# Kernel optimization log

Measured on AMD Instinct MI355X. Metric: run time of the kernel, lower is better.

The kernel has to match this reference:

```python
import jax, jax.numpy as jnp
import numpy as np
from jax import lax

NQ = 9          # num_qubits
K = 3           # basis_size
S = 16          # max_num_snapshots
H = 128         # hidden_size
B = 16          # batch
D = 2 ** NQ

# basis_reconstruction buffer = Pauli X, Y, Z (complex64), non-trainable
PAULI = jnp.array([[[0, 1], [1, 0]],
                   [[0, -1j], [1j, 0]],
                   [[1, 0], [0, -1]]], dtype=jnp.complex64)


def setup_inputs() -> dict:
    key = jax.random.key(0)
    ks = jax.random.split(key, 11)
    return {
        "snapshot": jax.random.normal(ks[0], (B, NQ), jnp.float32),
        "basis_comp_vector": jax.random.uniform(ks[1], (B, NQ, K), dtype=jnp.float32),
        "rho": jax.random.normal(ks[2], (B, 2) + (2,) * NQ, jnp.float32),
        "h0": jax.random.normal(ks[3], (B, H), jnp.float32),
        "c0": jax.random.normal(ks[4], (B, H), jnp.float32),
        "W_ih": jax.random.normal(ks[5], (4 * H, NQ + NQ * K), jnp.float32) * 0.1,
        "W_hh": jax.random.normal(ks[6], (4 * H, H), jnp.float32) * 0.1,
        "b_ih": jax.random.normal(ks[7], (4 * H,), jnp.float32) * 0.1,
        "b_hh": jax.random.normal(ks[8], (4 * H,), jnp.float32) * 0.1,
        "Wp": jax.random.normal(ks[9], (NQ, K, H), jnp.float32) * 0.1,
        "bp": jax.random.normal(ks[10], (NQ, K), jnp.float32) * 0.1,
    }


def _lstm_cell(x, h, c, W_ih, W_hh, b_ih, b_hh):
    g = x @ W_ih.T + h @ W_hh.T + b_ih + b_hh
    i, f, gg, o = jnp.split(g, 4, axis=-1)  # torch gate order i,f,g,o
    i, f, o = jax.nn.sigmoid(i), jax.nn.sigmoid(f), jax.nn.sigmoid(o)
    c = f * c + i * jnp.tanh(gg)
    return o * jnp.tanh(c), c


def _apply_1q(psi, M, i):
    """Apply per-batch 2x2 matrix M [B,2,2] to qubit i of psi [B]+[2]*NQ."""
    psi = jnp.moveaxis(psi, 1 + i, 1)
    sh = psi.shape
    out = jnp.einsum('bij,bjr->bir', M, psi.reshape(sh[0], 2, -1))
    return jnp.moveaxis(out.reshape(sh), 1, 1 + i)


def _take_snapshots(psi, a):
    """Vectorized take_snapshot: psi [B]+[2]*NQ complex, a [B,NQ,K] real (sqrt of probs).
    For each qubit build psi_plus/psi_minus projectors, record expectation
    s = <P+> - <P-> and collapse onto the (normalized) plus branch."""
    axs = tuple(range(1, NQ + 1))
    zeros = jnp.zeros(psi.shape[0], jnp.float32)
    ss = []
    for i in range(NQ):
        a1, a2, a3 = a[:, i, 0], a[:, i, 1], a[:, i, 2]
        an = jnp.sqrt(a1 * a1 + a2 * a2 + a3 * a3)
        nrm = 1.0 / jnp.sqrt(2.0 * an * (a3 + an))
        pp = jnp.stack([lax.complex(a3 + an, zeros), lax.complex(a1, a2)], axis=-1) * nrm[:, None]
        pm = jnp.stack([lax.complex(-a1, a2), lax.complex(a3 + an, zeros)], axis=-1) * nrm[:, None]
        Pp = pp[:, :, None] * jnp.conj(pp)[:, None, :]  # [B,2,2]
        Pm = pm[:, :, None] * jnp.conj(pm)[:, None, :]
        psi_p = _apply_1q(psi, Pp, i)
        psi_m = _apply_1q(psi, Pm, i)
        prob_p = jnp.sum(psi_p.real ** 2 + psi_p.imag ** 2, axis=axs)
        prob_m = jnp.sum(psi_m.real ** 2 + psi_m.imag ** 2, axis=axs)
        ss.append(prob_p - prob_m)
        psi = psi_p / jnp.sqrt(prob_p).reshape((-1,) + (1,) * NQ)  # collapse
    return jnp.stack(ss, axis=1)  # [B,NQ]


def _bkron(A, Bm):
    b, m, n = A.shape
    p, q = Bm.shape[1], Bm.shape[2]
    return (A[:, :, None, :, None] * Bm[:, None, :, None, :]).reshape(b, m * p, n * q)


def _forward(snapshot, basis_comp_vector, rho, h0, c0, W_ih, W_hh, b_ih, b_hh, Wp, bp):
    b = snapshot.shape[0]
    psi = lax.complex(rho[:, 0], rho[:, 1])  # [B]+[2]*NQ pure state
    x = jnp.concatenate([snapshot, basis_comp_vector.reshape(b, -1)], axis=-1)
    inputs = [x]
    h, c = h0, c0
    for _ in range(S - 1):
        h, c = _lstm_cell(x, h, c, W_ih, W_hh, b_ih, b_hh)
        probs = jax.nn.softmax(jnp.einsum('bh,nkh->bnk', h, Wp) + bp, axis=-1)
        amps = jnp.sqrt(probs)  # [B,NQ,K]
        snap = _take_snapshots(psi, amps)
        x = jnp.concatenate([snap, amps.reshape(b, -1)], axis=-1)
        inputs.append(x)
    # classical-shadow reconstruction, summed over snapshots
    I2 = jnp.eye(2, dtype=jnp.complex64)
    acc = jnp.zeros((b, D, D), jnp.complex64)
    last_bv = None
    for x in inputs:
        shadow = x[:, :NQ]                                   # [B,NQ]
        bv = x[:, NQ:].reshape(b, NQ, K)
        last_bv = bv
        basis = jnp.einsum('bnk,kij->bnij', bv.astype(jnp.complex64), PAULI)
        rho_q = (I2 + shadow[:, :, None, None].astype(jnp.complex64) * basis * 3.0) / 2.0
        r = rho_q[:, 0]
        for iq in range(1, NQ):
            r = _bkron(r, rho_q[:, iq])
        acc = acc + r
    rho_rec = acc / S
    out = jnp.stack([rho_rec.real, rho_rec.imag], axis=1)  # [B,2,D,D]
    return out, last_bv


def reference(snapshot, basis_comp_vector, rho, h0, c0, W_ih, W_hh, b_ih, b_hh, Wp, bp):
    return _forward(snapshot, basis_comp_vector, rho, h0, c0,
                    W_ih, W_hh, b_ih, b_hh, Wp, bp)
```

## Files before the change

### kernel.cpp

```cpp
#include <hip/hip_runtime.h>
#include <math.h>

#define NQ 9
#define KK 3
#define S 16
#define H 128
#define BB 16
#define D 512
#define DD (D*D)

__device__ __forceinline__ float sigf(float x){ return 1.f/(1.f + __expf(-x)); }

#define DPP_ADD(x, ctrl, rmask) \
  x += __int_as_float(__builtin_amdgcn_update_dpp(0, __float_as_int(x), ctrl, rmask, 0xf, false))

__device__ __forceinline__ float wave_red_sum(float x) {
  DPP_ADD(x, 0x111, 0xf);
  DPP_ADD(x, 0x112, 0xf);
  DPP_ADD(x, 0x114, 0xf);
  DPP_ADD(x, 0x118, 0xf);
  DPP_ADD(x, 0x142, 0xa);
  DPP_ADD(x, 0x143, 0xc);
  return __int_as_float(__builtin_amdgcn_readlane(__float_as_int(x), 63));
}
#define RL(v, l) __int_as_float(__builtin_amdgcn_readlane(__float_as_int(v), (l)))
#define DPP_ROR(x, n) \
  __int_as_float(__builtin_amdgcn_update_dpp(0, __float_as_int(x), 0x120 + (n), 0xf, 0xf, false))

__global__ __launch_bounds__(512, 2)
void seq_kernel(const float* __restrict__ snapshot,
                const float* __restrict__ bcv,
                const float* __restrict__ rho,
                const float* __restrict__ h0,
                const float* __restrict__ c0,
                const float* __restrict__ W_ih,
                const float* __restrict__ W_hh,
                const float* __restrict__ b_ih,
                const float* __restrict__ b_hh,
                const float* __restrict__ Wp,
                const float* __restrict__ bp,
                float4* __restrict__ mats,
                float* __restrict__ last_bv)
{
  const int b    = blockIdx.x;
  const int tid  = threadIdx.x;
  const int lane = tid & 63;
  const int w    = tid >> 6;

  __shared__ __align__(16) float xh[164];
  __shared__ float gbuf[512];
  __shared__ float prj[27];

  float4 wih[9], whh[32];
  {
    const float4* wi = (const float4*)(W_ih + tid*36);
    #pragma unroll
    for (int k = 0; k < 9; ++k) wih[k] = wi[k];
    const float4* wh = (const float4*)(W_hh + tid*H);
    #pragma unroll
    for (int k = 0; k < 32; ++k) whh[k] = wh[k];
  }
  const float bias = b_ih[tid] + b_hh[tid];
  float2 wpv[4]; float bpv[4];
  #pragma unroll
  for (int i = 0; i < 4; ++i) {
    int u = w + 8*i;
    if (u < 27) { wpv[i] = *(const float2*)(Wp + u*H + 2*lane); bpv[i] = bp[u]; }
    else        { wpv[i] = make_float2(0.f, 0.f); bpv[i] = 0.f; }
  }

  float cc0 = c0[b*H + 2*lane], cc1 = c0[b*H + 2*lane + 1];

  float pr0[8], pi0[8], norm0 = 0.f;
  if (w == 0) {
    #pragma unroll
    for (int j = 0; j < 8; ++j) {
      pr0[j] = rho[b*1024 + j*64 + lane];
      pi0[j] = rho[b*1024 + 512 + j*64 + lane];
    }
    float ls = 0.f;
    #pragma unroll
    for (int j = 0; j < 8; ++j) ls += pr0[j]*pr0[j] + pi0[j]*pi0[j];
    norm0 = wave_red_sum(ls);
  }

  if (tid < 128) xh[36 + tid] = h0[b*H + tid];
  if (tid < NQ)  xh[tid]      = snapshot[b*NQ + tid];
  if (tid < 27)  xh[NQ + tid] = bcv[b*27 + tid];
  __syncthreads();

  if (tid < NQ) {
    float s = xh[tid], v0 = xh[9+tid*3], v1 = xh[9+tid*3+1], v2 = xh[9+tid*3+2];
    mats[(b*S + 0)*NQ + tid] = make_float4(
        0.5f*(1.f + 3.f*s*v2), 1.5f*s*v0, -1.5f*s*v1, 0.5f*(1.f - 3.f*s*v2));
  }

  for (int t = 1; t < S; ++t) {
    {
      const float4* x4 = (const float4*)xh;
      float g0 = bias, g1 = 0.f, g2 = 0.f, g3 = 0.f;
      #pragma unroll
      for (int k = 0; k < 9; ++k) {
        float4 wv = wih[k], xv = x4[k];
        g0 += wv.x*xv.x; g1 += wv.y*xv.y; g2 += wv.z*xv.z; g3 += wv.w*xv.w;
      }
      #pragma unroll
      for (int k = 0; k < 32; ++k) {
        float4 wv = whh[k], xv = x4[9 + k];
        g0 += wv.x*xv.x; g1 += wv.y*xv.y; g2 += wv.z*xv.z; g3 += wv.w*xv.w;
      }
      gbuf[tid] = (g0 + g1) + (g2 + g3);
    }
    __syncthreads();

    float h0v, h1v;
    {
      float2 gI = *(const float2*)(gbuf + 2*lane);
      float2 gF = *(const float2*)(gbuf + 128 + 2*lane);
      float2 gG = *(const float2*)(gbuf + 256 + 2*lane);
      float2 gO = *(const float2*)(gbuf + 384 + 2*lane);
      cc0 = sigf(gF.x)*cc0 + sigf(gI.x)*tanhf(gG.x);
      cc1 = sigf(gF.y)*cc1 + sigf(gI.y)*tanhf(gG.y);
      h0v = sigf(gO.x)*tanhf(cc0);
      h1v = sigf(gO.y)*tanhf(cc1);
    }
    if (w == 1) *(float2*)(xh + 36 + 2*lane) = make_float2(h0v, h1v);

    #pragma unroll
    for (int i = 0; i < 4; ++i) {
      float p = wave_red_sum(wpv[i].x*h0v + wpv[i].y*h1v);
      int u = w + 8*i;
      if (u < 27 && lane == 0) prj[u] = p + bpv[i];
    }
    __syncthreads();

    if (w == 0) {
      float a1 = 0.f, a2 = 0.f, a3 = 0.f;
      float k0v = 0.f, k1rv = 0.f, k1iv = 0.f;
      if (lane < NQ) {
        float l0 = prj[lane*3], l1 = prj[lane*3+1], l2 = prj[lane*3+2];
        float mx = fmaxf(l0, fmaxf(l1, l2));
        float e0 = __expf(l0 - mx), e1 = __expf(l1 - mx), e2 = __expf(l2 - mx);
        float inv = 1.f/(e0 + e1 + e2);
        a1 = sqrtf(e0*inv); a2 = sqrtf(e1*inv); a3 = sqrtf(e2*inv);
        float an = sqrtf(a1*a1 + a2*a2 + a3*a3);
        float t3 = a3 + an;
        float n1 = 1.f/sqrtf(2.f*an*t3);
        k0v = n1*t3; k1rv = n1*a1; k1iv = -n1*a2;
      }
      float part[9];

      float r4[4], i4[4];
      {
        const float K0 = RL(k0v,0), K1r = RL(k1rv,0), K1i = RL(k1iv,0);
        float lp = 0.f;
        #pragma unroll
        for (int j = 0; j < 4; ++j) {
          r4[j] = K0*pr0[j] + K1r*pr0[j+4] - K1i*pi0[j+4];
          i4[j] = K0*pi0[j] + K1r*pi0[j+4] + K1i*pr0[j+4];
          lp += r4[j]*r4[j] + i4[j]*i4[j];
        }
        part[0] = lp;
      }
      float r2[2], i2[2];
      {
        const float K0 = RL(k0v,1), K1r = RL(k1rv,1), K1i = RL(k1iv,1);
        float lp = 0.f;
        #pragma unroll
        for (int j = 0; j < 2; ++j) {
          r2[j] = K0*r4[j] + K1r*r4[j+2] - K1i*i4[j+2];
          i2[j] = K0*i4[j] + K1r*i4[j+2] + K1i*r4[j+2];
          lp += r2[j]*r2[j] + i2[j]*i2[j];
        }
        part[1] = lp;
      }
      float wr, wi_;
      {
        const float K0 = RL(k0v,2), K1r = RL(k1rv,2), K1i = RL(k1iv,2);
        wr  = K0*r2[0] + K1r*r2[1] - K1i*i2[1];
        wi_ = K0*i2[0] + K1r*i2[1] + K1i*r2[1];
        part[2] = wr*wr + wi_*wi_;
      }
      #pragma unroll
      for (int q = 3; q < 5; ++q) {
        const int half = 32 >> (q - 3);
        const float K0 = RL(k0v,q), K1r = RL(k1rv,q), K1i = RL(k1iv,q);
        float pr = __shfl(wr,  lane + half, 64);
        float pi = __shfl(wi_, lane + half, 64);
        float nr = K0*wr  + K1r*pr - K1i*pi;
        float ni = K0*wi_ + K1r*pi + K1i*pr;
        wr = nr; wi_ = ni;
        part[q] = (lane < half) ? (nr*nr + ni*ni) : 0.f;
      }
      #pragma unroll
      for (int q = 5; q < NQ; ++q) {
        const int half = 32 >> (q - 3);
        const float K0 = RL(k0v,q), K1r = RL(k1rv,q), K1i = RL(k1iv,q);
        float pr, pi;
        if      (q == 5) { pr = DPP_ROR(wr, 8);  pi = DPP_ROR(wi_, 8);  }
        else if (q == 6) { pr = DPP_ROR(wr, 12); pi = DPP_ROR(wi_, 12); }
        else if (q == 7) { pr = DPP_ROR(wr, 14); pi = DPP_ROR(wi_, 14); }
        else             { pr = DPP_ROR(wr, 15); pi = DPP_ROR(wi_, 15); }
        float nr = K0*wr  + K1r*pr - K1i*pi;
        float ni = K0*wi_ + K1r*pi + K1i*pr;
        wr = nr; wi_ = ni;
        part[q] = (lane < half) ? (nr*nr + ni*ni) : 0.f;
      }
      float L[9];
      #pragma unroll
      for (int q = 0; q < NQ; ++q) L[q] = wave_red_sum(part[q]);
      float sv = 2.f*L[0] - norm0;
      #pragma unroll
      for (int q = 1; q < NQ; ++q) {
        float r = 2.f*L[q]/L[q-1] - 1.f;
        sv = (lane == q) ? r : sv;
      }
      if (lane < NQ) {
        xh[lane] = sv;
        xh[9 + lane*3]     = a1;
        xh[9 + lane*3 + 1] = a2;
        xh[9 + lane*3 + 2] = a3;
        mats[(b*S + t)*NQ + lane] = make_float4(
            0.5f*(1.f + 3.f*sv*a3), 1.5f*sv*a1,
            -1.5f*sv*a2,            0.5f*(1.f - 3.f*sv*a3));
      }
    }
    __syncthreads();
  }

  if (tid < 27) last_bv[b*27 + tid] = xh[9 + tid];
}

__device__ __forceinline__ void herm_entry(float4 m, int rb, int cb, float& er, float& ei) {
  if (rb == 0) { if (cb == 0) { er = m.x; ei = 0.f; } else { er = m.y; ei = m.z; } }
  else         { if (cb == 0) { er = m.y; ei = -m.z; } else { er = m.w; ei = 0.f; } }
}

__global__ __launch_bounds__(512, 2)
void kron_kernel(const float4* __restrict__ mats_g, float* __restrict__ out)
{
  const int b   = blockIdx.y;
  const int bm  = blockIdx.x;
  const int tid = threadIdx.x;
  const int rTp = bm >> 3;
  const int rg  = bm & 7;

  __shared__ float4 matsh[S*NQ];
  __shared__ float2 top[S][2][16];
  __shared__ __align__(16) float2 bot[4][S][32];

  if (tid < S*NQ) matsh[tid] = mats_g[b*S*NQ + tid];
  __syncthreads();

  {
    int t = tid >> 5, rTi = (tid >> 4) & 1, cT = tid & 15;
    int rT = rTp*2 + rTi;
    float re = 1.f, im = 0.f;
    #pragma unroll
    for (int q = 0; q < 4; ++q) {
      int rb = (rT >> (3 - q)) & 1, cb = (cT >> (3 - q)) & 1;
      float er, ei; herm_entry(matsh[t*NQ + q], rb, cb, er, ei);
      float nr = re*er - im*ei; im = re*ei + im*er; re = nr;
    }
    top[t][rTi][cT] = make_float2(re, im);
  }
  {
    int r_ = tid >> 7, t_ = (tid >> 3) & 15, cB0 = (tid & 7) << 2;
    int rB = rg*4 + r_;
    #pragma unroll
    for (int i = 0; i < 4; ++i) {
      int cB = cB0 + i;
      float re = 1.f, im = 0.f;
      #pragma unroll
      for (int q = 0; q < 5; ++q) {
        int rb = (rB >> (4 - q)) & 1, cb = (cB >> (4 - q)) & 1;
        float er, ei; herm_entry(matsh[t_*NQ + 4 + q], rb, cb, er, ei);
        float nr = re*er - im*ei; im = re*ei + im*er; re = nr;
      }
      bot[r_][t_][cB] = make_float2(re, im);
    }
  }
  __syncthreads();

  const int rb = tid >> 7;
  const int c0 = (tid & 127) << 2;
  const int cT = c0 >> 5, cB = c0 & 31;
  float4 a0r = make_float4(0,0,0,0), a0i = make_float4(0,0,0,0);
  float4 a1r = make_float4(0,0,0,0), a1i = make_float4(0,0,0,0);
  #pragma unroll
  for (int t = 0; t < S; ++t) {
    float4 b01 = *(const float4*)&bot[rb][t][cB];
    float4 b23 = *(const float4*)&bot[rb][t][cB + 2];
    float2 tA = top[t][0][cT];
    float2 tB = top[t][1][cT];
    a0r.x += tA.x*b01.x - tA.y*b01.y;  a0i.x += tA.x*b01.y + tA.y*b01.x;
    a0r.y += tA.x*b01.z - tA.y*b01.w;  a0i.y += tA.x*b01.w + tA.y*b01.z;
    a0r.z += tA.x*b23.x - tA.y*b23.y;  a0i.z += tA.x*b23.y + tA.y*b23.x;
    a0r.w += tA.x*b23.z - tA.y*b23.w;  a0i.w += tA.x*b23.w + tA.y*b23.z;
    a1r.x += tB.x*b01.x - tB.y*b01.y;  a1i.x += tB.x*b01.y + tB.y*b01.x;
    a1r.y += tB.x*b01.z - tB.y*b01.w;  a1i.y += tB.x*b01.w + tB.y*b01.z;
    a1r.z += tB.x*b23.x - tB.y*b23.y;  a1i.z += tB.x*b23.y + tB.y*b23.x;
    a1r.w += tB.x*b23.z - tB.y*b23.w;  a1i.w += tB.x*b23.w + tB.y*b23.z;
  }
  const float invS = 1.f/16.f;
  a0r.x*=invS; a0r.y*=invS; a0r.z*=invS; a0r.w*=invS;
  a0i.x*=invS; a0i.y*=invS; a0i.z*=invS; a0i.w*=invS;
  a1r.x*=invS; a1r.y*=invS; a1r.z*=invS; a1r.w*=invS;
  a1i.x*=invS; a1i.y*=invS; a1i.z*=invS; a1i.w*=invS;
  const int rowA = (rTp*2)*32 + rg*4 + rb;
  const int rowB = rowA + 32;
  size_t baseA = ((size_t)b*2)*DD + (size_t)rowA*D + c0;
  size_t baseB = ((size_t)b*2)*DD + (size_t)rowB*D + c0;
  *(float4*)(out + baseA)      = a0r;
  *(float4*)(out + baseA + DD) = a0i;
  *(float4*)(out + baseB)      = a1r;
  *(float4*)(out + baseB + DD) = a1i;
}

extern "C" void kernel_launch(void* const* d_in, const int* in_sizes, int n_in,
                              void* d_out, int out_size, void* d_ws, size_t ws_size,
                              hipStream_t stream) {
  const float* snapshot = (const float*)d_in[0];
  const float* bcv      = (const float*)d_in[1];
  const float* rho      = (const float*)d_in[2];
  const float* h0       = (const float*)d_in[3];
  const float* c0       = (const float*)d_in[4];
  const float* W_ih     = (const float*)d_in[5];
  const float* W_hh     = (const float*)d_in[6];
  const float* b_ih     = (const float*)d_in[7];
  const float* b_hh     = (const float*)d_in[8];
  const float* Wp       = (const float*)d_in[9];
  const float* bp       = (const float*)d_in[10];

  float*  out     = (float*)d_out;
  float4* mats    = (float4*)d_ws;
  float*  last_bv = out + (size_t)BB*2*DD;

  seq_kernel<<<BB, 512, 0, stream>>>(snapshot, bcv, rho, h0, c0,
                                     W_ih, W_hh, b_ih, b_hh, Wp, bp,
                                     mats, last_bv);

  dim3 grid(64, BB);
  kron_kernel<<<grid, 512, 0, stream>>>(mats, out);
}
```

Measured before the change: 171.5 us.

## Overlap LSTM recurrent matvec with snapshot step, use fast math and nontemporal stores

The recurrent W_hh·h product is now computed in registers from h broadcast with readlane and moved to the end of each step, so it overlaps with wave 0's snapshot work instead of waiting behind a shared-memory round trip. tanh, reciprocals and rsqrt are replaced with fast approximate intrinsics, which reduces accuracy somewhat. The kron kernel rebalances the bottom-factor construction so each thread builds entries along a contiguous index, and writes its output with nontemporal stores to avoid cache pollution. The exp-based tanh can overflow for large inputs.

```diff
diff --git a/kernel.cpp b/kernel.cpp
--- a/kernel.cpp
+++ b/kernel.cpp
@@ -9,7 +9,15 @@
 #define D 512
 #define DD (D*D)
 
+typedef float vfloat4 __attribute__((ext_vector_type(4)));
+
 __device__ __forceinline__ float sigf(float x){ return 1.f/(1.f + __expf(-x)); }
+__device__ __forceinline__ float tanhfast(float x){
+  float e = __expf(2.f*x);
+  return 1.f - 2.f/(e + 1.f);
+}
+#define RCP(x)  __builtin_amdgcn_rcpf(x)
+#define RSQ(x)  __builtin_amdgcn_rsqf(x)
 
 #define DPP_ADD(x, ctrl, rmask) \
   x += __int_as_float(__builtin_amdgcn_update_dpp(0, __float_as_int(x), ctrl, rmask, 0xf, false))
@@ -47,7 +55,7 @@
   const int lane = tid & 63;
   const int w    = tid >> 6;
 
-  __shared__ __align__(16) float xh[164];
+  __shared__ __align__(16) float xh[36];
   __shared__ float gbuf[512];
   __shared__ float prj[27];
 
@@ -70,6 +78,7 @@
   }
 
   float cc0 = c0[b*H + 2*lane], cc1 = c0[b*H + 2*lane + 1];
+  float h0v = h0[b*H + 2*lane], h1v = h0[b*H + 2*lane + 1];
 
   float pr0[8], pi0[8], norm0 = 0.f;
   if (w == 0) {
@@ -84,48 +93,49 @@
     norm0 = wave_red_sum(ls);
   }
 
-  if (tid < 128) xh[36 + tid] = h0[b*H + tid];
   if (tid < NQ)  xh[tid]      = snapshot[b*NQ + tid];
   if (tid < 27)  xh[NQ + tid] = bcv[b*27 + tid];
-  __syncthreads();
-
   if (tid < NQ) {
-    float s = xh[tid], v0 = xh[9+tid*3], v1 = xh[9+tid*3+1], v2 = xh[9+tid*3+2];
+    float s  = snapshot[b*NQ + tid];
+    float v0 = bcv[b*27 + tid*3];
+    float v1 = bcv[b*27 + tid*3 + 1];
+    float v2 = bcv[b*27 + tid*3 + 2];
     mats[(b*S + 0)*NQ + tid] = make_float4(
         0.5f*(1.f + 3.f*s*v2), 1.5f*s*v0, -1.5f*s*v1, 0.5f*(1.f - 3.f*s*v2));
   }
+
+  float ghh = bias;
+  #pragma unroll
+  for (int j = 0; j < 32; ++j) {
+    float4 wv = whh[j];
+    ghh += wv.x*RL(h0v, 2*j)     + wv.y*RL(h1v, 2*j)
+         + wv.z*RL(h0v, 2*j + 1) + wv.w*RL(h1v, 2*j + 1);
+  }
+  __syncthreads();
 
   for (int t = 1; t < S; ++t) {
     {
       const float4* x4 = (const float4*)xh;
-      float g0 = bias, g1 = 0.f, g2 = 0.f, g3 = 0.f;
+      float g0 = ghh, g1 = 0.f, g2 = 0.f, g3 = 0.f;
       #pragma unroll
       for (int k = 0; k < 9; ++k) {
         float4 wv = wih[k], xv = x4[k];
         g0 += wv.x*xv.x; g1 += wv.y*xv.y; g2 += wv.z*xv.z; g3 += wv.w*xv.w;
       }
-      #pragma unroll
-      for (int k = 0; k < 32; ++k) {
-        float4 wv = whh[k], xv = x4[9 + k];
-        g0 += wv.x*xv.x; g1 += wv.y*xv.y; g2 += wv.z*xv.z; g3 += wv.w*xv.w;
-      }
       gbuf[tid] = (g0 + g1) + (g2 + g3);
     }
     __syncthreads();
 
-    float h0v, h1v;
     {
       float2 gI = *(const float2*)(gbuf + 2*lane);
       float2 gF = *(const float2*)(gbuf + 128 + 2*lane);
       float2 gG = *(const float2*)(gbuf + 256 + 2*lane);
       float2 gO = *(const float2*)(gbuf + 384 + 2*lane);
-      cc0 = sigf(gF.x)*cc0 + sigf(gI.x)*tanhf(gG.x);
-      cc1 = sigf(gF.y)*cc1 + sigf(gI.y)*tanhf(gG.y);
-      h0v = sigf(gO.x)*tanhf(cc0);
-      h1v = sigf(gO.y)*tanhf(cc1);
-    }
-    if (w == 1) *(float2*)(xh + 36 + 2*lane) = make_float2(h0v, h1v);
-
+      cc0 = sigf(gF.x)*cc0 + sigf(gI.x)*tanhfast(gG.x);
+      cc1 = sigf(gF.y)*cc1 + sigf(gI.y)*tanhfast(gG.y);
+      h0v = sigf(gO.x)*tanhfast(cc0);
+      h1v = sigf(gO.y)*tanhfast(cc1);
+    }
     #pragma unroll
     for (int i = 0; i < 4; ++i) {
       float p = wave_red_sum(wpv[i].x*h0v + wpv[i].y*h1v);
@@ -141,11 +151,11 @@
         float l0 = prj[lane*3], l1 = prj[lane*3+1], l2 = prj[lane*3+2];
         float mx = fmaxf(l0, fmaxf(l1, l2));
         float e0 = __expf(l0 - mx), e1 = __expf(l1 - mx), e2 = __expf(l2 - mx);
-        float inv = 1.f/(e0 + e1 + e2);
+        float inv = RCP(e0 + e1 + e2);
         a1 = sqrtf(e0*inv); a2 = sqrtf(e1*inv); a3 = sqrtf(e2*inv);
         float an = sqrtf(a1*a1 + a2*a2 + a3*a3);
         float t3 = a3 + an;
-        float n1 = 1.f/sqrtf(2.f*an*t3);
+        float n1 = RSQ(2.f*an*t3);
         k0v = n1*t3; k1rv = n1*a1; k1iv = -n1*a2;
       }
       float part[9];
@@ -212,7 +222,7 @@
       float sv = 2.f*L[0] - norm0;
       #pragma unroll
       for (int q = 1; q < NQ; ++q) {
-        float r = 2.f*L[q]/L[q-1] - 1.f;
+        float r = 2.f*L[q]*RCP(L[q-1]) - 1.f;
         sv = (lane == q) ? r : sv;
       }
       if (lane < NQ) {
@@ -225,6 +235,17 @@
             -1.5f*sv*a2,            0.5f*(1.f - 3.f*sv*a3));
       }
     }
+
+    if (t < S - 1) {
+      float g = bias;
+      #pragma unroll
+      for (int j = 0; j < 32; ++j) {
+        float4 wv = whh[j];
+        g += wv.x*RL(h0v, 2*j)     + wv.y*RL(h1v, 2*j)
+           + wv.z*RL(h0v, 2*j + 1) + wv.w*RL(h1v, 2*j + 1);
+      }
+      ghh = g;
+    }
     __syncthreads();
   }
 
@@ -234,6 +255,11 @@
 __device__ __forceinline__ void herm_entry(float4 m, int rb, int cb, float& er, float& ei) {
   if (rb == 0) { if (cb == 0) { er = m.x; ei = 0.f; } else { er = m.y; ei = m.z; } }
   else         { if (cb == 0) { er = m.y; ei = -m.z; } else { er = m.w; ei = 0.f; } }
+}
+
+__device__ __forceinline__ void nt_store4(float* p, float x, float y, float z, float w) {
+  vfloat4 v; v.x = x; v.y = y; v.z = z; v.w = w;
+  __builtin_nontemporal_store(v, (vfloat4*)p);
 }
 
 __global__ __launch_bounds__(512, 2)
@@ -264,21 +290,19 @@
     }
     top[t][rTi][cT] = make_float2(re, im);
   }
-  {
-    int r_ = tid >> 7, t_ = (tid >> 3) & 15, cB0 = (tid & 7) << 2;
+  #pragma unroll
+  for (int i = 0; i < 4; ++i) {
+    int n  = tid + 512*i;
+    int r_ = n >> 9, t_ = (n >> 5) & 15, cB = n & 31;
     int rB = rg*4 + r_;
-    #pragma unroll
-    for (int i = 0; i < 4; ++i) {
-      int cB = cB0 + i;
-      float re = 1.f, im = 0.f;
-      #pragma unroll
-      for (int q = 0; q < 5; ++q) {
-        int rb = (rB >> (4 - q)) & 1, cb = (cB >> (4 - q)) & 1;
-        float er, ei; herm_entry(matsh[t_*NQ + 4 + q], rb, cb, er, ei);
-        float nr = re*er - im*ei; im = re*ei + im*er; re = nr;
-      }
-      bot[r_][t_][cB] = make_float2(re, im);
-    }
+    float re = 1.f, im = 0.f;
+    #pragma unroll
+    for (int q = 0; q < 5; ++q) {
+      int rb = (rB >> (4 - q)) & 1, cb = (cB >> (4 - q)) & 1;
+      float er, ei; herm_entry(matsh[t_*NQ + 4 + q], rb, cb, er, ei);
+      float nr = re*er - im*ei; im = re*ei + im*er; re = nr;
+    }
+    bot[r_][t_][cB] = make_float2(re, im);
   }
   __syncthreads();
 
@@ -303,18 +327,14 @@
     a1r.w += tB.x*b23.z - tB.y*b23.w;  a1i.w += tB.x*b23.w + tB.y*b23.z;
   }
   const float invS = 1.f/16.f;
-  a0r.x*=invS; a0r.y*=invS; a0r.z*=invS; a0r.w*=invS;
-  a0i.x*=invS; a0i.y*=invS; a0i.z*=invS; a0i.w*=invS;
-  a1r.x*=invS; a1r.y*=invS; a1r.z*=invS; a1r.w*=invS;
-  a1i.x*=invS; a1i.y*=invS; a1i.z*=invS; a1i.w*=invS;
   const int rowA = (rTp*2)*32 + rg*4 + rb;
   const int rowB = rowA + 32;
   size_t baseA = ((size_t)b*2)*DD + (size_t)rowA*D + c0;
   size_t baseB = ((size_t)b*2)*DD + (size_t)rowB*D + c0;
-  *(float4*)(out + baseA)      = a0r;
-  *(float4*)(out + baseA + DD) = a0i;
-  *(float4*)(out + baseB)      = a1r;
-  *(float4*)(out + baseB + DD) = a1i;
+  nt_store4(out + baseA,      a0r.x*invS, a0r.y*invS, a0r.z*invS, a0r.w*invS);
+  nt_store4(out + baseA + DD, a0i.x*invS, a0i.y*invS, a0i.z*invS, a0i.w*invS);
+  nt_store4(out + baseB,      a1r.x*invS, a1r.y*invS, a1r.z*invS, a1r.w*invS);
+  nt_store4(out + baseB + DD, a1i.x*invS, a1i.y*invS, a1i.z*invS, a1i.w*invS);
 }
 
 extern "C" void kernel_launch(void* const* d_in, const int* in_sizes, int n_in,
```

Result: faster. 155.4 us (-9.4%).
